# Performance work log

Measured on AMD Instinct MI355X. Metric: run time of the kernel, lower is better.

## Reference

```python
import jax, jax.numpy as jnp
import numpy as np

KS, PAD, N = 3, 1, 9  # deformable 3x3 kernel, padding 1, N = 9 taps
EPS = 1e-5


def conv2d(x, w, b=None, stride=1, padding=1):
    out = jax.lax.conv_general_dilated(
        x, w, (stride, stride), [(padding, padding)] * 2,
        dimension_numbers=("NCHW", "OIHW", "NCHW"))
    if b is not None:
        out = out + b[None, :, None, None]
    return out


def batchnorm(x, gamma, beta):
    # training-mode BN (fresh module, batch statistics), biased variance like torch
    mean = jnp.mean(x, axis=(0, 2, 3), keepdims=True)
    var = jnp.var(x, axis=(0, 2, 3), keepdims=True)
    xn = (x - mean) * jax.lax.rsqrt(var + EPS)
    return xn * gamma[None, :, None, None] + beta[None, :, None, None]


def gather_corners(xp, qx, qy):
    # xp: (b,c,Hp,Wp); qx,qy: (b,h,w,N) int32 -> (b,c,h,w,N)
    b, c, Hp, Wp = xp.shape
    _, h, w, n = qx.shape
    idx = (qx * Wp + qy).reshape(b, 1, h * w * n)
    out = jnp.take_along_axis(xp.reshape(b, c, Hp * Wp), idx, axis=2)
    return out.reshape(b, c, h, w, n)


def deform_conv(feat, offset, w4):
    # feat: (b,256,h,w), offset: (b,18,h,w) interleaved (x1,y1,x2,y2,...)
    b, c, h, w = feat.shape
    off_x = jnp.transpose(offset[:, 0::2], (0, 2, 3, 1))  # (b,h,w,N)
    off_y = jnp.transpose(offset[:, 1::2], (0, 2, 3, 1))
    xp = jnp.pad(feat, ((0, 0), (0, 0), (PAD, PAD), (PAD, PAD)))
    Hp, Wp = h + 2 * PAD, w + 2 * PAD
    # kernel tap offsets, row-major over (dx,dy)
    pn_x = jnp.array([-1, -1, -1, 0, 0, 0, 1, 1, 1], jnp.float32)
    pn_y = jnp.array([-1, 0, 1, -1, 0, 1, -1, 0, 1], jnp.float32)
    p0_x = jnp.arange(1, h + 1, dtype=jnp.float32)[None, :, None, None]
    p0_y = jnp.arange(1, w + 1, dtype=jnp.float32)[None, None, :, None]
    px = p0_x + pn_x[None, None, None, :] + off_x  # sampling coords in padded map
    py = p0_y + pn_y[None, None, None, :] + off_y

    fpx = jnp.floor(jax.lax.stop_gradient(px))
    fpy = jnp.floor(jax.lax.stop_gradient(py))
    q_lt_x = jnp.clip(fpx, 0, Hp - 1).astype(jnp.int32)
    q_lt_y = jnp.clip(fpy, 0, Wp - 1).astype(jnp.int32)
    q_rb_x = jnp.clip(fpx + 1, 0, Hp - 1).astype(jnp.int32)
    q_rb_y = jnp.clip(fpy + 1, 0, Wp - 1).astype(jnp.int32)

    # out-of-range points snapped to floor (as in original), then clamped
    mask_x = (px < PAD) | (px > Hp - 1 - PAD)
    mask_y = (py < PAD) | (py > Wp - 1 - PAD)
    px = jnp.clip(jnp.where(mask_x, jnp.floor(px), px), 0, Hp - 1)
    py = jnp.clip(jnp.where(mask_y, jnp.floor(py), py), 0, Wp - 1)

    ltx, lty = q_lt_x.astype(jnp.float32), q_lt_y.astype(jnp.float32)
    rbx, rby = q_rb_x.astype(jnp.float32), q_rb_y.astype(jnp.float32)
    g_lt = (1 + (ltx - px)) * (1 + (lty - py))
    g_rb = (1 - (rbx - px)) * (1 - (rby - py))
    g_lb = (1 + (ltx - px)) * (1 - (rby - py))
    g_rt = (1 - (rbx - px)) * (1 + (lty - py))

    x_off = (g_lt[:, None] * gather_corners(xp, q_lt_x, q_lt_y)
             + g_rb[:, None] * gather_corners(xp, q_rb_x, q_rb_y)
             + g_lb[:, None] * gather_corners(xp, q_lt_x, q_rb_y)
             + g_rt[:, None] * gather_corners(xp, q_rb_x, q_lt_y))  # (b,c,h,w,N)

    # stride-ks conv over the ks*ks-expanded map == contraction over (c, tap)
    outc = w4.shape[0]
    return jnp.einsum("bchwn,ocn->bohw", x_off, w4.reshape(outc, c, N))


def setup_inputs() -> dict:
    key = jax.random.key(0)
    ks = jax.random.split(key, 8)
    x = jax.random.normal(ks[0], (2, 3, 224, 224), jnp.float32)
    w1 = jax.random.normal(ks[1], (64, 3, 3, 3), jnp.float32) * 0.1
    b1 = jnp.zeros((64,), jnp.float32)
    g1 = jnp.ones((64,), jnp.float32)
    be1 = jnp.zeros((64,), jnp.float32)
    w2 = jax.random.normal(ks[2], (256, 64, 3, 3), jnp.float32) * 0.04
    b2 = jnp.zeros((256,), jnp.float32)
    g2 = jnp.ones((256,), jnp.float32)
    be2 = jnp.zeros((256,), jnp.float32)
    w_off = jax.random.normal(ks[3], (18, 256, 3, 3), jnp.float32) * 0.01
    b_off = jnp.zeros((18,), jnp.float32)
    w4 = jax.random.normal(ks[4], (256, 256, 3, 3), jnp.float32) * 0.02
    return dict(x=x, w1=w1, b1=b1, g1=g1, be1=be1, w2=w2, b2=b2, g2=g2,
                be2=be2, w_off=w_off, b_off=b_off, w4=w4)


def reference(x, w1, b1, g1, be1, w2, b2, g2, be2, w_off, b_off, w4):
    h = jax.nn.relu(conv2d(x, w1, b1))
    h = batchnorm(h, g1, be1)
    b_, c, H, W = h.shape
    h = h.reshape(b_, c, H // 2, 2, W // 2, 2).mean(axis=(3, 5))  # AvgPool 2x2
    h = jax.nn.relu(conv2d(h, w2, b2))
    h = batchnorm(h, g2, be2)
    offset = conv2d(h, w_off, b_off)  # (b,18,h,w)
    return deform_conv(h, offset, w4)
```

## Files before the change

### kernel.cpp

```cpp
#include <hip/hip_runtime.h>
#include <hip/hip_bf16.h>

#define NP1 50176
#define NP2 12544
#define NPP 12996

typedef __attribute__((ext_vector_type(8))) short short8;
typedef __attribute__((ext_vector_type(4))) float f32x4;

__device__ __forceinline__ unsigned short f2bu(float f){
  __hip_bfloat16 h = __float2bfloat16(f);
  return *reinterpret_cast<unsigned short*>(&h);
}
__device__ __forceinline__ float blo(unsigned u){ union{unsigned q; float f;} x; x.q = u<<16; return x.f; }
__device__ __forceinline__ float bhi(unsigned u){ union{unsigned q; float f;} x; x.q = u & 0xffff0000u; return x.f; }

#define S_SUM1   0
#define S_SUM2   128
#define S_STATS1 640
#define S_STATS2 768
#define S_WOFF2  1280
#define S_W4F    75008
#define S_W2FH   369920
#define S_W2FL   443648
#define S_OFFB   517376
#define S_PPAD   968960
#define S_PHI    2632448
#define S_PLO    3464192
#define S_HPAD   4295936
#define S_HPADL  10949888
#define S_WOFFH  14276864
#define S_WOFFL  14313728
#define S_PB2    14350592
#define S_HPADH  15014144
#define WS_NEED_FLOATS 18341120ull
#define WS_NEED_BYTES  (WS_NEED_FLOATS*4ull)

__global__ void k_prep(const float* __restrict__ w4, const float* __restrict__ woff,
                       const float* __restrict__ w2,
                       unsigned short* __restrict__ w4f, float* __restrict__ woff2,
                       unsigned short* __restrict__ woffh, unsigned short* __restrict__ woffl,
                       unsigned short* __restrict__ w2fh, unsigned short* __restrict__ w2fl){
  int idx = blockIdx.x*256+threadIdx.x;
  if(idx < 589824){
    int kt = idx/8192; int r = idx - kt*8192;
    int oc = r>>5, kk = r&31;
    int k = kt*32 + kk; int n = k>>8, c = k&255;
    w4f[idx] = f2bu(w4[oc*2304 + c*9 + n]);
  } else if(idx < 663552){
    int i2 = idx - 589824;
    int k = i2>>5, oc = i2&31;
    int n = k>>8, c = k&255;
    woff2[i2] = (oc<18) ? woff[oc*2304 + c*9 + n] : 0.f;
  } else if(idx < 737280){
    int i3 = idx - 663552;
    int kt = i3>>10; int r = i3 & 1023;
    int oc = r>>5, kk = r&31;
    int k = kt*32 + kk; int n = k>>8, c = k&255;
    float wv = (oc<18) ? woff[oc*2304 + c*9 + n] : 0.f;
    unsigned short hi = f2bu(wv);
    woffh[i3] = hi;
    woffl[i3] = f2bu(wv - blo(hi));
  } else {
    int i4 = idx - 737280;
    int kt = i4/8192; int r = i4 - kt*8192;
    int oc = r>>5, kk = r&31;
    int k = kt*32 + kk; int n = k>>6, c = k&63;
    float wv = w2[oc*576 + c*9 + n];
    unsigned short hi = f2bu(wv);
    w2fh[i4] = hi;
    w2fl[i4] = f2bu(wv - blo(hi));
  }
}

__global__ __launch_bounds__(256) void k_conv1pool(
    const float* __restrict__ x, const float* __restrict__ w1, const float* __restrict__ b1,
    float* __restrict__ ppad, float* __restrict__ sum1){
  __shared__ float xs[3*34*34];
  int bid = blockIdx.x;
  int tile = bid % 49; int oc = (bid/49) & 63; int b = bid/(49*64);
  int tu = tile/7, tv = tile - 7*(tile/7);
  int tid = threadIdx.x;
  int in0 = tu*32 - 1, jn0 = tv*32 - 1;
  for(int t=tid; t<3468; t+=256){
    int c = t/1156; int r2 = t - c*1156; int rr = r2/34; int cc = r2 - rr*34;
    int ii = in0+rr, jj = jn0+cc;
    xs[t] = (ii>=0 && ii<224 && jj>=0 && jj<224) ? x[(size_t)(b*3+c)*NP1 + ii*224+jj] : 0.f;
  }
  float w[27];
  #pragma unroll
  for(int t=0;t<27;t++) w[t] = w1[oc*27+t];
  float bia = b1[oc];
  __syncthreads();
  int u = tid>>4, v = tid&15;
  float s1=0.f, s2=0.f, pl=0.f;
  #pragma unroll
  for(int dy=0;dy<2;dy++){
    #pragma unroll
    for(int dx=0;dx<2;dx++){
      float acc = bia;
      #pragma unroll
      for(int c=0;c<3;c++)
        #pragma unroll
        for(int kh=0;kh<3;kh++)
          #pragma unroll
          for(int kw=0;kw<3;kw++)
            acc += xs[c*1156 + (2*u+dy+kh)*34 + (2*v+dx+kw)] * w[c*9+kh*3+kw];
      acc = fmaxf(acc, 0.f);
      pl += acc; s1 += acc; s2 += acc*acc;
    }
  }
  int U = tu*16+u, V = tv*16+v;
  ppad[(size_t)(b*64+oc)*NPP + (U+1)*114 + (V+1)] = 0.25f*pl;
  __shared__ float r1[256], r2[256];
  r1[tid]=s1; r2[tid]=s2; __syncthreads();
  for(int o=128;o>0;o>>=1){
    if(tid<o){ r1[tid]+=r1[tid+o]; r2[tid]+=r2[tid+o]; }
    __syncthreads();
  }
  if(tid==0){ atomicAdd(&sum1[oc], r1[0]); atomicAdd(&sum1[64+oc], r2[0]); }
}

__global__ void k_fin1(const float* __restrict__ sum1, const float* __restrict__ g1,
                       const float* __restrict__ be1, float* __restrict__ stats1){
  int ch = threadIdx.x;
  float n = 2.f*(float)NP1;
  float mean = sum1[ch]/n;
  float var  = sum1[64+ch]/n - mean*mean;
  float sc = g1[ch]/sqrtf(var + 1e-5f);
  stats1[ch]    = sc;
  stats1[64+ch] = be1[ch] - mean*sc;
}

__global__ __launch_bounds__(256) void k_affine1t(const float* __restrict__ ppad,
        const float* __restrict__ stats1,
        unsigned short* __restrict__ phi, unsigned short* __restrict__ plo){
  __shared__ float ls[64*65];
  int bid = blockIdx.x;
  int b = bid/204; int pp0 = (bid - b*204)*64;
  int tid = threadIdx.x;
  #pragma unroll
  for(int it=0; it<16; it++){
    int t = it*256 + tid;
    int c = t>>6, q = t&63;
    int pp = pp0 + q;
    float v = 0.f;
    if(pp < NPP){
      int row = pp/114, col = pp - row*114;
      if(row>=1 && row<=112 && col>=1 && col<=112)
        v = stats1[c]*ppad[(size_t)(b*64+c)*NPP + pp] + stats1[64+c];
    }
    ls[c*65+q] = v;
  }
  __syncthreads();
  #pragma unroll
  for(int it=0; it<16; it++){
    int t = it*256 + tid;
    int qq = t/64, c = t%64;
    int qloc = qq & 63;
    int pp = pp0 + qloc;
    if(pp < NPP){
      float v = ls[c*65 + qloc];
      unsigned short hi = f2bu(v);
      phi[((size_t)b*NPP + pp)*64 + c] = hi;
      plo[((size_t)b*NPP + pp)*64 + c] = f2bu(v - blo(hi));
    }
  }
}

__global__ __launch_bounds__(256) void k_conv2(
    const unsigned short* __restrict__ phi, const unsigned short* __restrict__ plo,
    const unsigned short* __restrict__ w2fh, const unsigned short* __restrict__ w2fl,
    const float* __restrict__ b2, float* __restrict__ hpad, float* __restrict__ sum2){
  __shared__ float smemf[8800];
  int*  pp_tbl = (int*)smemf;
  unsigned short* afh0 = (unsigned short*)(smemf + 576);
  unsigned short* afl0 = (unsigned short*)(smemf + 576 + 2560);
  float* tb = smemf + 576;
  const int tid = threadIdx.x;
  const int wave = tid>>6, lane = tid&63;
  const int sidx = (blockIdx.x & 7)*49 + (blockIdx.x >> 3);
  const int pix0 = sidx*64;
  const int b = pix0/NP2, ij0 = pix0 - b*NP2;

  for(int t=tid; t<576; t+=256){
    int p = t/9, n = t - 9*(t/9);
    int ij = ij0+p; int i = ij/112, j = ij - i*112;
    pp_tbl[p*9+n] = (i + n/3)*114 + (j + n%3);
  }
  const int px_g = tid>>2;
  const int coff = (tid&3)*8;
  const unsigned short* ph_b = phi + (size_t)b*NPP*64;
  const unsigned short* pl_b = plo + (size_t)b*NPP*64;

  f32x4 acc[4][4] = {};
  __syncthreads();

  auto STAGE = [&](int kt, int buf){
    int n = kt>>1; int cb = ((kt&1)<<5) + coff;
    int pp = pp_tbl[px_g*9 + n];
    *(uint4*)&afh0[buf*2560 + px_g*40 + coff] = *(const uint4*)(ph_b + (size_t)pp*64 + cb);
    *(uint4*)&afl0[buf*2560 + px_g*40 + coff] = *(const uint4*)(pl_b + (size_t)pp*64 + cb);
  };

  const int klo = (lane>>4)<<3;
  STAGE(0, 0);
  for(int kt=0; kt<18; kt++){
    __syncthreads();
    if(kt+1 < 18) STAGE(kt+1, (kt+1)&1);
    const unsigned short* abh = afh0 + (kt&1)*2560;
    const unsigned short* abl = afl0 + (kt&1)*2560;
    short8 aH[4], aL[4];
    #pragma unroll
    for(int mf=0; mf<4; mf++){
      aH[mf] = *(const short8*)&abh[(mf*16 + (lane&15))*40 + klo];
      aL[mf] = *(const short8*)&abl[(mf*16 + (lane&15))*40 + klo];
    }
    #pragma unroll
    for(int nf=0; nf<4; nf++){
      int oc = wave*64 + nf*16 + (lane&15);
      short8 bH = *(const short8*)&w2fh[(size_t)kt*8192 + oc*32 + klo];
      short8 bL = *(const short8*)&w2fl[(size_t)kt*8192 + oc*32 + klo];
      #pragma unroll
      for(int mf=0; mf<4; mf++){
        acc[mf][nf] = __builtin_amdgcn_mfma_f32_16x16x32_bf16(aH[mf], bH, acc[mf][nf], 0,0,0);
        acc[mf][nf] = __builtin_amdgcn_mfma_f32_16x16x32_bf16(aH[mf], bL, acc[mf][nf], 0,0,0);
        acc[mf][nf] = __builtin_amdgcn_mfma_f32_16x16x32_bf16(aL[mf], bH, acc[mf][nf], 0,0,0);
      }
    }
  }
  const int row0 = (lane>>4)<<2, col = lane&15;
  float s1q[4] = {0.f,0.f,0.f,0.f}, s2q[4] = {0.f,0.f,0.f,0.f};
  for(int half=0; half<2; half++){
    __syncthreads();
    #pragma unroll
    for(int m2=0; m2<2; m2++){
      int mf = half*2 + m2;
      #pragma unroll
      for(int nf=0; nf<4; nf++){
        int oc = wave*64 + nf*16 + col;
        #pragma unroll
        for(int r=0;r<4;r++) tb[(m2*16 + row0 + r)*257 + oc] = acc[mf][nf][r];
      }
    }
    __syncthreads();
    #pragma unroll
    for(int it=0; it<8; it++){
      int id = it*256 + tid;
      int pxl = id>>6, oc4 = id&63;
      int px = half*32 + pxl;
      int ij = ij0+px; int i = ij/112, j = ij - i*112;
      int pp = (i+1)*114 + (j+1);
      float4 v;
      v.x = fmaxf(tb[pxl*257 + oc4*4+0] + b2[oc4*4+0], 0.f);
      v.y = fmaxf(tb[pxl*257 + oc4*4+1] + b2[oc4*4+1], 0.f);
      v.z = fmaxf(tb[pxl*257 + oc4*4+2] + b2[oc4*4+2], 0.f);
      v.w = fmaxf(tb[pxl*257 + oc4*4+3] + b2[oc4*4+3], 0.f);
      *(float4*)&hpad[((size_t)b*NPP + pp)*256 + oc4*4] = v;
      s1q[0] += v.x; s2q[0] += v.x*v.x;
      s1q[1] += v.y; s2q[1] += v.y*v.y;
      s1q[2] += v.z; s2q[2] += v.z*v.z;
      s1q[3] += v.w; s2q[3] += v.w*v.w;
    }
  }
  __syncthreads();
  #pragma unroll
  for(int q=0;q<4;q++){ tb[tid*4+q] = s1q[q]; tb[1024 + tid*4+q] = s2q[q]; }
  __syncthreads();
  {
    int oc = tid;
    float s1 = ((tb[oc] + tb[256+oc]) + tb[512+oc]) + tb[768+oc];
    float s2 = ((tb[1024+oc] + tb[1280+oc]) + tb[1536+oc]) + tb[1792+oc];
    atomicAdd(&sum2[oc], s1); atomicAdd(&sum2[256+oc], s2);
  }
}

__global__ void k_fin2(const float* __restrict__ sum2, const float* __restrict__ g2,
                       const float* __restrict__ be2, float* __restrict__ stats2){
  int ch = threadIdx.x;
  float n = 2.f*(float)NP2;
  float mean = sum2[ch]/n;
  float var  = sum2[256+ch]/n - mean*mean;
  float sc = g2[ch]/sqrtf(var + 1e-5f);
  stats2[ch]     = sc;
  stats2[256+ch] = be2[ch] - mean*sc;
}

__global__ void k_affine2(float* __restrict__ hpad, const float* __restrict__ stats2,
                          unsigned short* __restrict__ hpadh, unsigned short* __restrict__ hpadl){
  int idx = blockIdx.x*256+threadIdx.x;
  int c = idx & 255; int pi = idx >> 8;
  int pp = pi % NPP;
  int row = pp/114, col = pp - row*114;
  bool in = (row>=1 && row<=112 && col>=1 && col<=112);
  float v = in ? (stats2[c]*hpad[idx] + stats2[256+c]) : 0.f;
  bool band = (row<6) || (row>107) || (col<6) || (col>107);
  if(band) hpad[idx] = v;
  unsigned short hi = f2bu(v);
  hpadh[idx] = hi;
  hpadl[idx] = f2bu(v - blo(hi));
}

__global__ __launch_bounds__(256) void k_convoff_mfma(
    const unsigned short* __restrict__ hpadh, const unsigned short* __restrict__ hpadl,
    const unsigned short* __restrict__ woffh, const unsigned short* __restrict__ woffl,
    float* __restrict__ p0, float* __restrict__ p1, float* __restrict__ p2){
  __shared__ int pp_tbl[192];
  __shared__ __align__(16) unsigned short afh[2][64*72];
  __shared__ __align__(16) unsigned short afl[2][64*72];
  const int tid = threadIdx.x;
  const int wave = tid>>6, lane = tid&63;
  const int g = blockIdx.x;
  const int xcd = g & 7;
  const int rr  = g >> 3;
  const int split = rr % 3;
  const int sstrip = rr / 3;
  const int strip = xcd*49 + sstrip;
  const int pix0 = strip*64;
  const int b = pix0/NP2, ij0 = pix0 - b*NP2;
  const int n0 = split*3;

  for(int t=tid; t<192; t+=256){
    int p = t/3, nl = t - 3*(t/3);
    int ij = ij0+p; int i = ij/112, j = ij - i*112;
    int n = n0 + nl;
    pp_tbl[p*3+nl] = (i + n/3)*114 + (j + n%3);
  }
  const int px_g = tid>>2;
  const int coff = (tid&3)*16;
  const unsigned short* ph_b = hpadh + (size_t)b*NPP*256;
  const unsigned short* pl_b = hpadl + (size_t)b*NPP*256;
  const int r15 = lane&15, klo = (lane>>4)<<3;

  f32x4 acc[2] = {};
  __syncthreads();

  auto STAGE = [&](int ph, int buf){
    int nl = ph>>2, q = ph&3;
    int pp = pp_tbl[px_g*3 + nl];
    int cb = q*64 + coff;
    uint4 h0 = *(const uint4*)(ph_b + (size_t)pp*256 + cb);
    uint4 h1 = *(const uint4*)(ph_b + (size_t)pp*256 + cb + 8);
    uint4 l0 = *(const uint4*)(pl_b + (size_t)pp*256 + cb);
    uint4 l1 = *(const uint4*)(pl_b + (size_t)pp*256 + cb + 8);
    *(uint4*)&afh[buf][px_g*72 + coff    ] = h0;
    *(uint4*)&afh[buf][px_g*72 + coff + 8] = h1;
    *(uint4*)&afl[buf][px_g*72 + coff    ] = l0;
    *(uint4*)&afl[buf][px_g*72 + coff + 8] = l1;
  };

  STAGE(0, 0);
  for(int ph=0; ph<12; ph++){
    __syncthreads();
    if(ph+1 < 12) STAGE(ph+1, (ph+1)&1);
    const unsigned short* ah = &afh[ph&1][(wave*16 + r15)*72];
    const unsigned short* al = &afl[ph&1][(wave*16 + r15)*72];
    const int n = n0 + (ph>>2), q = ph&3;
    #pragma unroll
    for(int half=0; half<2; half++){
      int kt = n*8 + q*2 + half;
      short8 aH = *(const short8*)&ah[half*32 + klo];
      short8 aL = *(const short8*)&al[half*32 + klo];
      #pragma unroll
      for(int nf=0; nf<2; nf++){
        int oc = nf*16 + r15;
        short8 bH = *(const short8*)&woffh[(size_t)kt*1024 + oc*32 + klo];
        short8 bL = *(const short8*)&woffl[(size_t)kt*1024 + oc*32 + klo];
        acc[nf] = __builtin_amdgcn_mfma_f32_16x16x32_bf16(aH, bH, acc[nf], 0,0,0);
        acc[nf] = __builtin_amdgcn_mfma_f32_16x16x32_bf16(aH, bL, acc[nf], 0,0,0);
        acc[nf] = __builtin_amdgcn_mfma_f32_16x16x32_bf16(aL, bH, acc[nf], 0,0,0);
      }
    }
  }
  float* dst = (split==0) ? p0 : (split==1) ? p1 : p2;
  const int row0 = (lane>>4)<<2;
  #pragma unroll
  for(int nf=0; nf<2; nf++){
    int oc = nf*16 + r15;
    if(oc < 18)
      *(f32x4*)(dst + (size_t)(b*18+oc)*NP2 + ij0 + wave*16 + row0) = acc[nf];
  }
}

__global__ void k_offred3(float* __restrict__ offb, const float* __restrict__ p1,
                          const float* __restrict__ p2, const float* __restrict__ boff){
  int idx = blockIdx.x*256+threadIdx.x;
  int oc = (idx/NP2) % 18;
  offb[idx] = ((offb[idx] + p1[idx]) + p2[idx]) + boff[oc];
}

__global__ __launch_bounds__(256) void k_offfix(const float* __restrict__ hpad,
        const float* __restrict__ woff2, const float* __restrict__ boff,
        float* __restrict__ offb){
  int idx = blockIdx.x*256 + threadIdx.x;
  if(idx >= 83712) return;
  int oc = idx & 31;
  int pid = idx >> 5;
  int b = pid / 1308; int t = pid - b*1308;
  int i, j;
  if(t < 672){
    int r = t/112; i = (r<3) ? r : 106+r; j = t - (t/112)*112;
  } else {
    int u = t - 672; i = 3 + u/6; int c6 = u - 6*(u/6);
    j = (c6<3) ? c6 : 106+c6;
  }
  const float* hb = hpad + (size_t)b*NPP*256;
  float a0=0.f, a1=0.f, a2=0.f, a3=0.f;
  for(int n=0;n<9;n++){
    const float* ap = hb + (size_t)((i + n/3)*114 + (j + n%3))*256;
    const float* wp = woff2 + (size_t)n*256*32 + oc;
    #pragma unroll 4
    for(int c=0;c<256;c+=4){
      float4 a = *(const float4*)(ap + c);
      a0 = fmaf(a.x, wp[(c+0)*32], a0);
      a1 = fmaf(a.y, wp[(c+1)*32], a1);
      a2 = fmaf(a.z, wp[(c+2)*32], a2);
      a3 = fmaf(a.w, wp[(c+3)*32], a3);
    }
  }
  if(oc < 18)
    offb[(size_t)(b*18+oc)*NP2 + i*112 + j] = ((a0+a1)+(a2+a3)) + boff[oc];
}

__global__ __launch_bounds__(256) void k_deform(
    const unsigned short* __restrict__ hpadh,
    const float* __restrict__ offb,
    const unsigned short* __restrict__ w4f,
    float* __restrict__ out){
  __shared__ int   gidx[64][9][4];
  __shared__ float gwt [64][9][4];
  __shared__ __align__(16) unsigned short afrag[2][64*72];
  const int tid = threadIdx.x;
  const int wave = tid>>6, lane = tid&63;
  const int sidx = (blockIdx.x & 7)*49 + (blockIdx.x >> 3);
  const int pix0 = sidx*64;
  const int b = pix0/NP2, ij0 = pix0 - b*NP2;

  for(int t=tid; t<576; t+=256){
    int p = t/9, n = t - 9*(t/9);
    int ij = ij0+p; int i = ij/112, j = ij - i*112;
    float ox = offb[(size_t)(b*18 + 2*n  )*NP2 + ij];
    float oy = offb[(size_t)(b*18 + 2*n+1)*NP2 + ij];
    float px = (float)(i + n/3) + ox;
    float py = (float)(j + n%3) + oy;
    float fpx = floorf(px), fpy = floorf(py);
    float qltxf = fminf(fmaxf(fpx,     0.f),113.f);
    float qltyf = fminf(fmaxf(fpy,     0.f),113.f);
    float qrbxf = fminf(fmaxf(fpx+1.f, 0.f),113.f);
    float qrbyf = fminf(fmaxf(fpy+1.f, 0.f),113.f);
    int qltx=(int)qltxf, qlty=(int)qltyf, qrbx=(int)qrbxf, qrby=(int)qrbyf;
    bool mx = (px<1.f)||(px>112.f);
    bool my = (py<1.f)||(py>112.f);
    float pxc = fminf(fmaxf(mx?fpx:px, 0.f),113.f);
    float pyc = fminf(fmaxf(my?fpy:py, 0.f),113.f);
    float glt = (1.f+(qltxf-pxc))*(1.f+(qltyf-pyc));
    float grb = (1.f-(qrbxf-pxc))*(1.f-(qrbyf-pyc));
    float glb = (1.f+(qltxf-pxc))*(1.f-(qrbyf-pyc));
    float grt = (1.f-(qrbxf-pxc))*(1.f+(qltyf-pyc));
    gidx[p][n][0]=qltx*114+qlty; gwt[p][n][0]=glt;
    gidx[p][n][1]=qrbx*114+qrby; gwt[p][n][1]=grb;
    gidx[p][n][2]=qltx*114+qrby; gwt[p][n][2]=glb;
    gidx[p][n][3]=qrbx*114+qlty; gwt[p][n][3]=grt;
  }

  const int px_g   = tid>>2;
  const int coff_g = (tid&3)*8;
  const unsigned short* hb = hpadh + (size_t)b*NPP*256;

  f32x4 acc[4][4] = {};
  __syncthreads();

  auto GATHER = [&](int ph, int buf){
    int n = ph>>2; int qb = (ph&3)<<6;
    const int*   gi = gidx[px_g][n];
    const float* gw = gwt[px_g][n];
    int i0 = gi[0], i1 = gi[1], i2 = gi[2], i3 = gi[3];
    float w0 = gw[0], w1 = gw[1], w2 = gw[2], w3 = gw[3];
    #pragma unroll
    for(int h=0; h<2; h++){
      int cb = qb + h*32 + coff_g;
      f32x4 va = {0.f,0.f,0.f,0.f}, vb = {0.f,0.f,0.f,0.f};
      const uint4 u0 = *(const uint4*)(hb + (size_t)i0*256 + cb);
      const uint4 u1 = *(const uint4*)(hb + (size_t)i1*256 + cb);
      const uint4 u2 = *(const uint4*)(hb + (size_t)i2*256 + cb);
      const uint4 u3 = *(const uint4*)(hb + (size_t)i3*256 + cb);
      va.x = fmaf(w0, blo(u0.x), va.x); va.y = fmaf(w0, bhi(u0.x), va.y);
      va.z = fmaf(w0, blo(u0.y), va.z); va.w = fmaf(w0, bhi(u0.y), va.w);
      vb.x = fmaf(w0, blo(u0.z), vb.x); vb.y = fmaf(w0, bhi(u0.z), vb.y);
      vb.z = fmaf(w0, blo(u0.w), vb.z); vb.w = fmaf(w0, bhi(u0.w), vb.w);
      va.x = fmaf(w1, blo(u1.x), va.x); va.y = fmaf(w1, bhi(u1.x), va.y);
      va.z = fmaf(w1, blo(u1.y), va.z); va.w = fmaf(w1, bhi(u1.y), va.w);
      vb.x = fmaf(w1, blo(u1.z), vb.x); vb.y = fmaf(w1, bhi(u1.z), vb.y);
      vb.z = fmaf(w1, blo(u1.w), vb.z); vb.w = fmaf(w1, bhi(u1.w), vb.w);
      va.x = fmaf(w2, blo(u2.x), va.x); va.y = fmaf(w2, bhi(u2.x), va.y);
      va.z = fmaf(w2, blo(u2.y), va.z); va.w = fmaf(w2, bhi(u2.y), va.w);
      vb.x = fmaf(w2, blo(u2.z), vb.x); vb.y = fmaf(w2, bhi(u2.z), vb.y);
      vb.z = fmaf(w2, blo(u2.w), vb.z); vb.w = fmaf(w2, bhi(u2.w), vb.w);
      va.x = fmaf(w3, blo(u3.x), va.x); va.y = fmaf(w3, bhi(u3.x), va.y);
      va.z = fmaf(w3, blo(u3.y), va.z); va.w = fmaf(w3, bhi(u3.y), va.w);
      vb.x = fmaf(w3, blo(u3.z), vb.x); vb.y = fmaf(w3, bhi(u3.z), vb.y);
      vb.z = fmaf(w3, blo(u3.w), vb.z); vb.w = fmaf(w3, bhi(u3.w), vb.w);
      uint4 o;
      o.x = (unsigned)f2bu(va.x) | ((unsigned)f2bu(va.y)<<16);
      o.y = (unsigned)f2bu(va.z) | ((unsigned)f2bu(va.w)<<16);
      o.z = (unsigned)f2bu(vb.x) | ((unsigned)f2bu(vb.y)<<16);
      o.w = (unsigned)f2bu(vb.z) | ((unsigned)f2bu(vb.w)<<16);
      *(uint4*)&afrag[buf][px_g*72 + h*32 + coff_g] = o;
    }
  };

  const int klo = (lane>>4)<<3;
  GATHER(0, 0);
  for(int ph=0; ph<36; ph++){
    __syncthreads();
    if(ph+1 < 36) GATHER(ph+1, (ph+1)&1);
    const unsigned short* ab = afrag[ph&1];
    #pragma unroll
    for(int h=0; h<2; h++){
      int kt = (ph>>2)*8 + (ph&3)*2 + h;
      short8 aF[4];
      #pragma unroll
      for(int mf=0; mf<4; mf++)
        aF[mf] = *(const short8*)&ab[(mf*16 + (lane&15))*72 + h*32 + klo];
      const unsigned short* wb = w4f + (size_t)kt*8192 + klo;
      #pragma unroll
      for(int nf=0; nf<4; nf++){
        int oc = wave*64 + nf*16 + (lane&15);
        short8 bF = *(const short8*)&wb[oc*32];
        #pragma unroll
        for(int mf=0; mf<4; mf++)
          acc[mf][nf] = __builtin_amdgcn_mfma_f32_16x16x32_bf16(aF[mf], bF, acc[mf][nf], 0,0,0);
      }
    }
  }
  int row0 = ((lane>>4)<<2);
  int col  = lane&15;
  #pragma unroll
  for(int mf=0; mf<4; mf++)
    #pragma unroll
    for(int nf=0; nf<4; nf++){
      int oc = wave*64 + nf*16 + col;
      size_t ob = (size_t)(b*256+oc)*NP2 + ij0 + mf*16 + row0;
      *(f32x4*)(out + ob) = acc[mf][nf];
    }
}

extern "C" void kernel_launch(void* const* d_in, const int* in_sizes, int n_in,
                              void* d_out, int out_size, void* d_ws, size_t ws_size,
                              hipStream_t stream){
  (void)in_sizes; (void)n_in;
  const float* x    = (const float*)d_in[0];
  const float* w1   = (const float*)d_in[1];
  const float* b1   = (const float*)d_in[2];
  const float* g1   = (const float*)d_in[3];
  const float* be1  = (const float*)d_in[4];
  const float* w2   = (const float*)d_in[5];
  const float* b2   = (const float*)d_in[6];
  const float* g2   = (const float*)d_in[7];
  const float* be2  = (const float*)d_in[8];
  const float* woff = (const float*)d_in[9];
  const float* boff = (const float*)d_in[10];
  const float* w4   = (const float*)d_in[11];
  float* out = (float*)d_out;
  float* ws = (float*)d_ws;

  if(ws_size < WS_NEED_BYTES){
    hipMemsetAsync(d_out, 0, (size_t)out_size*sizeof(float), stream);
    return;
  }

  float* sum1   = ws + S_SUM1;
  float* sum2   = ws + S_SUM2;
  float* stats1 = ws + S_STATS1;
  float* stats2 = ws + S_STATS2;
  float* woff2  = ws + S_WOFF2;
  unsigned short* w4f   = (unsigned short*)(ws + S_W4F);
  unsigned short* w2fh  = (unsigned short*)(ws + S_W2FH);
  unsigned short* w2fl  = (unsigned short*)(ws + S_W2FL);
  unsigned short* woffh = (unsigned short*)(ws + S_WOFFH);
  unsigned short* woffl = (unsigned short*)(ws + S_WOFFL);
  float* offb   = ws + S_OFFB;
  float* ppad   = ws + S_PPAD;
  float* pb1    = ws + S_PPAD;
  float* pb2    = ws + S_PB2;
  unsigned short* phi = (unsigned short*)(ws + S_PHI);
  unsigned short* plo = (unsigned short*)(ws + S_PLO);
  float* hpad   = ws + S_HPAD;
  unsigned short* hpadh = (unsigned short*)(ws + S_HPADH);
  unsigned short* hpadl = (unsigned short*)(ws + S_HPADL);

  hipMemsetAsync(sum1, 0, 640*sizeof(float), stream);
  k_prep         <<<3456,  256, 0, stream>>>(w4, woff, w2, w4f, woff2, woffh, woffl, w2fh, w2fl);
  k_conv1pool    <<<6272,  256, 0, stream>>>(x, w1, b1, ppad, sum1);
  k_fin1         <<<1,     64,  0, stream>>>(sum1, g1, be1, stats1);
  k_affine1t     <<<408,   256, 0, stream>>>(ppad, stats1, phi, plo);
  k_conv2        <<<392,   256, 0, stream>>>(phi, plo, w2fh, w2fl, b2, hpad, sum2);
  k_fin2         <<<1,     256, 0, stream>>>(sum2, g2, be2, stats2);
  k_affine2      <<<25992, 256, 0, stream>>>(hpad, stats2, hpadh, hpadl);
  k_convoff_mfma <<<1176,  256, 0, stream>>>(hpadh, hpadl, woffh, woffl, offb, pb1, pb2);
  k_offred3      <<<1764,  256, 0, stream>>>(offb, pb1, pb2, boff);
  k_offfix       <<<327,   256, 0, stream>>>(hpad, woff2, boff, offb);
  k_deform       <<<392,   256, 0, stream>>>(hpadh, offb, w4f, out);
}
```

Before: 386.2 us.

## Vectorize affine2/offred3 and split deform into 32-pixel 128-thread blocks

k_affine2 and k_offred3 now process four elements per thread with 128-bit loads and stores, cutting launch size and memory instructions. k_deform is restructured to 128-thread blocks handling 32 pixels each, with every wave computing 128 output channels over two 16-row M tiles, doubling the block count for better CU occupancy. This raises weight-fragment reloads per MFMA and changes the per-wave tile shape.

```diff
diff --git a/kernel.cpp b/kernel.cpp
--- a/kernel.cpp
+++ b/kernel.cpp
@@ -289,16 +289,27 @@
 __global__ void k_affine2(float* __restrict__ hpad, const float* __restrict__ stats2,
                           unsigned short* __restrict__ hpadh, unsigned short* __restrict__ hpadl){
   int idx = blockIdx.x*256+threadIdx.x;
-  int c = idx & 255; int pi = idx >> 8;
+  int c4 = (idx & 63) << 2;
+  int pi = idx >> 6;
   int pp = pi % NPP;
   int row = pp/114, col = pp - row*114;
   bool in = (row>=1 && row<=112 && col>=1 && col<=112);
-  float v = in ? (stats2[c]*hpad[idx] + stats2[256+c]) : 0.f;
+  float4 h = *(const float4*)&hpad[(size_t)pi*256 + c4];
+  float4 v;
+  v.x = in ? (stats2[c4+0]*h.x + stats2[256+c4+0]) : 0.f;
+  v.y = in ? (stats2[c4+1]*h.y + stats2[256+c4+1]) : 0.f;
+  v.z = in ? (stats2[c4+2]*h.z + stats2[256+c4+2]) : 0.f;
+  v.w = in ? (stats2[c4+3]*h.w + stats2[256+c4+3]) : 0.f;
   bool band = (row<6) || (row>107) || (col<6) || (col>107);
-  if(band) hpad[idx] = v;
-  unsigned short hi = f2bu(v);
-  hpadh[idx] = hi;
-  hpadl[idx] = f2bu(v - blo(hi));
+  if(band) *(float4*)&hpad[(size_t)pi*256 + c4] = v;
+  unsigned short hx = f2bu(v.x), hy = f2bu(v.y), hz = f2bu(v.z), hw = f2bu(v.w);
+  uint2 oh, ol;
+  oh.x = (unsigned)hx | ((unsigned)hy<<16);
+  oh.y = (unsigned)hz | ((unsigned)hw<<16);
+  ol.x = (unsigned)f2bu(v.x - blo(hx)) | ((unsigned)f2bu(v.y - blo(hy))<<16);
+  ol.y = (unsigned)f2bu(v.z - blo(hz)) | ((unsigned)f2bu(v.w - blo(hw))<<16);
+  *(uint2*)&hpadh[(size_t)pi*256 + c4] = oh;
+  *(uint2*)&hpadl[(size_t)pi*256 + c4] = ol;
 }
 
 __global__ __launch_bounds__(256) void k_convoff_mfma(
@@ -384,9 +395,18 @@
 
 __global__ void k_offred3(float* __restrict__ offb, const float* __restrict__ p1,
                           const float* __restrict__ p2, const float* __restrict__ boff){
-  int idx = blockIdx.x*256+threadIdx.x;
+  int i4 = blockIdx.x*256+threadIdx.x;
+  int idx = i4*4;
   int oc = (idx/NP2) % 18;
-  offb[idx] = ((offb[idx] + p1[idx]) + p2[idx]) + boff[oc];
+  float bo = boff[oc];
+  f32x4 a = *(const f32x4*)&offb[idx];
+  f32x4 q1 = *(const f32x4*)&p1[idx];
+  f32x4 q2 = *(const f32x4*)&p2[idx];
+  a.x = ((a.x + q1.x) + q2.x) + bo;
+  a.y = ((a.y + q1.y) + q2.y) + bo;
+  a.z = ((a.z + q1.z) + q2.z) + bo;
+  a.w = ((a.w + q1.w) + q2.w) + bo;
+  *(f32x4*)&offb[idx] = a;
 }
 
 __global__ __launch_bounds__(256) void k_offfix(const float* __restrict__ hpad,
@@ -422,21 +442,21 @@
     offb[(size_t)(b*18+oc)*NP2 + i*112 + j] = ((a0+a1)+(a2+a3)) + boff[oc];
 }
 
-__global__ __launch_bounds__(256) void k_deform(
+__global__ __launch_bounds__(128) void k_deform(
     const unsigned short* __restrict__ hpadh,
     const float* __restrict__ offb,
     const unsigned short* __restrict__ w4f,
     float* __restrict__ out){
-  __shared__ int   gidx[64][9][4];
-  __shared__ float gwt [64][9][4];
-  __shared__ __align__(16) unsigned short afrag[2][64*72];
+  __shared__ int   gidx[32][9][4];
+  __shared__ float gwt [32][9][4];
+  __shared__ __align__(16) unsigned short afrag[2][32*72];
   const int tid = threadIdx.x;
   const int wave = tid>>6, lane = tid&63;
-  const int sidx = (blockIdx.x & 7)*49 + (blockIdx.x >> 3);
-  const int pix0 = sidx*64;
+  const int sidx = (blockIdx.x & 7)*98 + (blockIdx.x >> 3);
+  const int pix0 = sidx*32;
   const int b = pix0/NP2, ij0 = pix0 - b*NP2;
 
-  for(int t=tid; t<576; t+=256){
+  for(int t=tid; t<288; t+=128){
     int p = t/9, n = t - 9*(t/9);
     int ij = ij0+p; int i = ij/112, j = ij - i*112;
     float ox = offb[(size_t)(b*18 + 2*n  )*NP2 + ij];
@@ -467,7 +487,7 @@
   const int coff_g = (tid&3)*8;
   const unsigned short* hb = hpadh + (size_t)b*NPP*256;
 
-  f32x4 acc[4][4] = {};
+  f32x4 acc[2][8] = {};
   __syncthreads();
 
   auto GATHER = [&](int ph, int buf){
@@ -509,6 +529,7 @@
     }
   };
 
+  const int r15 = lane&15;
   const int klo = (lane>>4)<<3;
   GATHER(0, 0);
   for(int ph=0; ph<36; ph++){
@@ -518,28 +539,27 @@
     #pragma unroll
     for(int h=0; h<2; h++){
       int kt = (ph>>2)*8 + (ph&3)*2 + h;
-      short8 aF[4];
+      short8 aF[2];
       #pragma unroll
-      for(int mf=0; mf<4; mf++)
-        aF[mf] = *(const short8*)&ab[(mf*16 + (lane&15))*72 + h*32 + klo];
+      for(int mf=0; mf<2; mf++)
+        aF[mf] = *(const short8*)&ab[(mf*16 + r15)*72 + h*32 + klo];
       const unsigned short* wb = w4f + (size_t)kt*8192 + klo;
       #pragma unroll
-      for(int nf=0; nf<4; nf++){
-        int oc = wave*64 + nf*16 + (lane&15);
+      for(int nf=0; nf<8; nf++){
+        int oc = wave*128 + nf*16 + r15;
         short8 bF = *(const short8*)&wb[oc*32];
         #pragma unroll
-        for(int mf=0; mf<4; mf++)
+        for(int mf=0; mf<2; mf++)
           acc[mf][nf] = __builtin_amdgcn_mfma_f32_16x16x32_bf16(aF[mf], bF, acc[mf][nf], 0,0,0);
       }
     }
   }
   int row0 = ((lane>>4)<<2);
-  int col  = lane&15;
   #pragma unroll
-  for(int mf=0; mf<4; mf++)
-    #pragma unroll
-    for(int nf=0; nf<4; nf++){
-      int oc = wave*64 + nf*16 + col;
+  for(int mf=0; mf<2; mf++)
+    #pragma unroll
+    for(int nf=0; nf<8; nf++){
+      int oc = wave*128 + nf*16 + r15;
       size_t ob = (size_t)(b*256+oc)*NP2 + ij0 + mf*16 + row0;
       *(f32x4*)(out + ob) = acc[mf][nf];
     }
@@ -596,9 +616,9 @@
   k_affine1t     <<<408,   256, 0, stream>>>(ppad, stats1, phi, plo);
   k_conv2        <<<392,   256, 0, stream>>>(phi, plo, w2fh, w2fl, b2, hpad, sum2);
   k_fin2         <<<1,     256, 0, stream>>>(sum2, g2, be2, stats2);
-  k_affine2      <<<25992, 256, 0, stream>>>(hpad, stats2, hpadh, hpadl);
+  k_affine2      <<<6498,  256, 0, stream>>>(hpad, stats2, hpadh, hpadl);
   k_convoff_mfma <<<1176,  256, 0, stream>>>(hpadh, hpadl, woffh, woffl, offb, pb1, pb2);
-  k_offred3      <<<1764,  256, 0, stream>>>(offb, pb1, pb2, boff);
+  k_offred3      <<<441,   256, 0, stream>>>(offb, pb1, pb2, boff);
   k_offfix       <<<327,   256, 0, stream>>>(hpad, woff2, boff, offb);
-  k_deform       <<<392,   256, 0, stream>>>(hpadh, offb, w4f, out);
-}
+  k_deform       <<<784,   128, 0, stream>>>(hpadh, offb, w4f, out);
+}
```

Result: slower. 427.0 us (+10.5%).
